# Kernel optimization log

Measured on AMD Instinct MI355X. Metric: run time of the kernel, lower is better.

Reference implementation:

```python
import jax, jax.numpy as jnp
import numpy as np

N_NODES = 100000


def _glorot(key, shape):
    fan_in, fan_out = shape
    lim = (6.0 / (fan_in + fan_out)) ** 0.5
    return jax.random.uniform(key, shape, jnp.float32, -lim, lim)


def setup_inputs() -> dict:
    key = jax.random.key(0)
    ks = jax.random.split(key, 16)
    E = 1600000
    IN, H, OUT = 32, 48, 32
    f = jax.random.normal(ks[0], (N_NODES, IN), jnp.float32)
    edge_index = jax.random.randint(ks[1], (2, E), 0, N_NODES, jnp.int64)
    # layer 1: theta IN->H, phi H->H
    Wt1 = _glorot(ks[2], (IN, H)); bt1 = jnp.zeros((H,), jnp.float32)
    Wp1 = _glorot(ks[3], (H, H));  bp1 = jnp.zeros((H,), jnp.float32)
    # layer 2: theta H->H, phi H->H
    Wt2 = _glorot(ks[4], (H, H)); bt2 = jnp.zeros((H,), jnp.float32)
    Wp2 = _glorot(ks[5], (H, H)); bp2 = jnp.zeros((H,), jnp.float32)
    # layer 3: theta H->OUT, phi OUT->OUT
    Wt3 = _glorot(ks[6], (H, OUT)); bt3 = jnp.zeros((OUT,), jnp.float32)
    Wp3 = _glorot(ks[7], (OUT, OUT)); bp3 = jnp.zeros((OUT,), jnp.float32)
    return {"f": f, "edge_index": edge_index,
            "Wt1": Wt1, "bt1": bt1, "Wp1": Wp1, "bp1": bp1,
            "Wt2": Wt2, "bt2": bt2, "Wp2": Wp2, "bp2": bp2,
            "Wt3": Wt3, "bt3": bt3, "Wp3": Wp3, "bp3": bp3}


def _triconv(f, src, dst, Wt, bt, Wp, bp):
    # message: linear_theta(f_i - f_j), i = target (dst), j = source (src)
    msg = (f[dst] - f[src]) @ Wt + bt          # [E, C_out]
    agg = jax.ops.segment_sum(msg, dst, num_segments=N_NODES)  # sum aggr
    return agg @ Wp + bp                        # linear_phi


def reference(f, edge_index, Wt1, bt1, Wp1, bp1, Wt2, bt2, Wp2, bp2, Wt3, bt3, Wp3, bp3):
    src, dst = edge_index[0], edge_index[1]
    h = jax.nn.relu(_triconv(f, src, dst, Wt1, bt1, Wp1, bp1))
    h = jax.nn.relu(_triconv(h, src, dst, Wt2, bt2, Wp2, bp2))
    out = jax.nn.softmax(_triconv(h, src, dst, Wt3, bt3, Wp3, bp3), axis=-1)
    return out
```

## Files before the change

### kernel.cpp

```cpp
#include <hip/hip_runtime.h>


#define SHIFT 9
#define SPAN 512
#define MAXB 256
#define CHUNK 4096


__global__ void k_detect(const unsigned int* __restrict__ ew,
                         int* __restrict__ flag, int* __restrict__ bcount) {
  int t = threadIdx.x;
  bcount[t] = 0;
  unsigned int v = 0;
#pragma unroll
  for (int j = 0; j < 4; ++j) v |= ew[2 * (t * 4 + j) + 1];
  __shared__ unsigned int red[256];
  red[t] = v;
  __syncthreads();
  for (int s = 128; s > 0; s >>= 1) {
    if (t < s) red[t] |= red[t + s];
    __syncthreads();
  }
  if (t == 0) flag[0] = (red[0] == 0u) ? 1 : 0;
}

__global__ void k_bcount(const void* __restrict__ edges,
                         const int* __restrict__ flag,
                         int* __restrict__ bcount, int E) {
  __shared__ int cnt[MAXB];
  int t = threadIdx.x;
  cnt[t] = 0;
  __syncthreads();
  int base = blockIdx.x * CHUNK;
  if (flag[0]) {
    const long long* p = (const long long*)edges;
#pragma unroll
    for (int j = 0; j < CHUNK / 256; ++j) {
      int idx = base + j * 256 + t;
      if (idx < E) atomicAdd(&cnt[((int)p[E + idx]) >> SHIFT], 1);
    }
  } else {
    const int* p = (const int*)edges;
#pragma unroll
    for (int j = 0; j < CHUNK / 256; ++j) {
      int idx = base + j * 256 + t;
      if (idx < E) atomicAdd(&cnt[p[E + idx] >> SHIFT], 1);
    }
  }
  __syncthreads();
  if (cnt[t]) atomicAdd(&bcount[t], cnt[t]);
}

__global__ void k_bscan(const int* __restrict__ bcount, int* __restrict__ bbase,
                        int* __restrict__ bcursor, int* __restrict__ offs,
                        int NB, int N, int E) {
  __shared__ int lds[MAXB];
  int t = threadIdx.x;
  int v = (t < NB) ? bcount[t] : 0;
  lds[t] = v;
  __syncthreads();
  for (int off = 1; off < MAXB; off <<= 1) {
    int add = (t >= off) ? lds[t - off] : 0;
    __syncthreads();
    lds[t] += add;
    __syncthreads();
  }
  int ex = lds[t] - v;
  bbase[t] = ex;
  bcursor[t] = ex;
  if (t == MAXB - 1) bbase[MAXB] = lds[t];
  if (t == 0) offs[N] = E;
}

__global__ void k_bin(const void* __restrict__ edges,
                      const int* __restrict__ flag, int* __restrict__ bcursor,
                      unsigned int* __restrict__ binned, int E) {
  __shared__ unsigned int pk[CHUNK];
  __shared__ unsigned char bk[CHUNK];
  __shared__ int cnt[MAXB], bb[MAXB], cnt2[MAXB];
  int t = threadIdx.x;
  cnt[t] = 0;
  cnt2[t] = 0;
  __syncthreads();
  int base = blockIdx.x * CHUNK;
  if (flag[0]) {
    const long long* p = (const long long*)edges;
#pragma unroll
    for (int j = 0; j < CHUNK / 256; ++j) {
      int li = j * 256 + t, idx = base + li;
      if (idx < E) {
        int s = (int)p[idx];
        int d = (int)p[E + idx];
        int b = d >> SHIFT;
        pk[li] = ((unsigned)(d & (SPAN - 1)) << 17) | (unsigned)s;
        bk[li] = (unsigned char)b;
        atomicAdd(&cnt[b], 1);
      }
    }
  } else {
    const int* p = (const int*)edges;
#pragma unroll
    for (int j = 0; j < CHUNK / 256; ++j) {
      int li = j * 256 + t, idx = base + li;
      if (idx < E) {
        int s = p[idx];
        int d = p[E + idx];
        int b = d >> SHIFT;
        pk[li] = ((unsigned)(d & (SPAN - 1)) << 17) | (unsigned)s;
        bk[li] = (unsigned char)b;
        atomicAdd(&cnt[b], 1);
      }
    }
  }
  __syncthreads();
  if (cnt[t]) bb[t] = atomicAdd(&bcursor[t], cnt[t]);
  __syncthreads();
#pragma unroll
  for (int j = 0; j < CHUNK / 256; ++j) {
    int li = j * 256 + t, idx = base + li;
    if (idx < E) {
      int b = bk[li];
      int r = atomicAdd(&cnt2[b], 1);
      binned[bb[b] + r] = pk[li];
    }
  }
}

__launch_bounds__(256) __global__
void k_bcsr(const unsigned int* __restrict__ binned,
            const int* __restrict__ bbase, int* __restrict__ offs,
            int* __restrict__ csr, int N) {
  __shared__ int deg[SPAN];
  __shared__ int gs[128];
  __shared__ int cur[SPAN];
  int b = blockIdx.x;
  int t = threadIdx.x;
  deg[t] = 0;
  deg[t + 256] = 0;
  __syncthreads();
  int base = bbase[b];
  int cnt = bbase[b + 1] - base;
  for (int e = t; e < cnt; e += 256)
    atomicAdd(&deg[binned[base + e] >> 17], 1);
  __syncthreads();
  if (t < 128) gs[t] = deg[4 * t] + deg[4 * t + 1] + deg[4 * t + 2] + deg[4 * t + 3];
  __syncthreads();
  for (int off = 1; off < 128; off <<= 1) {
    int add = (t < 128 && t >= off) ? gs[t - off] : 0;
    __syncthreads();
    if (t < 128) gs[t] += add;
    __syncthreads();
  }
  int nodeBase = b << SHIFT;
  if (t < 128) {
    int run = (t == 0) ? 0 : gs[t - 1];
#pragma unroll
    for (int j = 0; j < 4; ++j) {
      int li = 4 * t + j;
      cur[li] = run;
      int node = nodeBase + li;
      if (node < N) offs[node] = base + run;
      run += deg[li];
    }
  }
  __syncthreads();
  for (int e = t; e < cnt; e += 256) {
    unsigned int v = binned[base + e];
    int ld = v >> 17;
    int pos = atomicAdd(&cur[ld], 1);
    csr[base + pos] = (int)(v & 0x1FFFFu);
  }
}

template <int CIN, int COUT, int ACT>
__launch_bounds__(256) __global__
void k_layer(const float* __restrict__ hin, float* __restrict__ hout,
             const int* __restrict__ offs, const int* __restrict__ csr,
             const float* __restrict__ Wt, const float* __restrict__ bt,
             const float* __restrict__ Wp, const float* __restrict__ bp,
             int n) {
  constexpr int NPB = 64;
  constexpr int CH1 = CIN / 4;
  constexpr int NV1 = CH1 / 4;
  constexpr int CH2 = COUT / 4;

  __shared__ float Wtl[CIN * COUT];
  __shared__ float Wpl[COUT * COUT];
  __shared__ float btl[COUT];
  __shared__ float bpl[COUT];
  __shared__ float Tl[NPB][CIN + 4];
  __shared__ float o1l[NPB][COUT + 4];

  int t = threadIdx.x;
  for (int i = t; i < CIN * COUT; i += 256) Wtl[i] = Wt[i];
  for (int i = t; i < COUT * COUT; i += 256) Wpl[i] = Wp[i];
  if (t < COUT) {
    btl[t] = bt[t];
    bpl[t] = bp[t];
  }
  __syncthreads();

  int ln = t >> 2;
  int g = t & 3;
  int node = blockIdx.x * NPB + ln;
  bool valid = node < n;
  int start = valid ? offs[node] : 0;
  int end = valid ? offs[node + 1] : 0;
  float degf = (float)(end - start);

  const int c0 = g * CH1;
  const float* hc = hin + c0;
  float acc[CH1];
#pragma unroll
  for (int j = 0; j < CH1; ++j) acc[j] = 0.f;

  int k = start;
  for (; k + 3 < end; k += 4) {
    int s0 = csr[k], s1 = csr[k + 1], s2 = csr[k + 2], s3 = csr[k + 3];
    float4 v0[NV1], v1[NV1], v2[NV1], v3[NV1];
    const float4* r0 = reinterpret_cast<const float4*>(hc + (size_t)s0 * CIN);
    const float4* r1 = reinterpret_cast<const float4*>(hc + (size_t)s1 * CIN);
    const float4* r2 = reinterpret_cast<const float4*>(hc + (size_t)s2 * CIN);
    const float4* r3 = reinterpret_cast<const float4*>(hc + (size_t)s3 * CIN);
#pragma unroll
    for (int q = 0; q < NV1; ++q) v0[q] = r0[q];
#pragma unroll
    for (int q = 0; q < NV1; ++q) v1[q] = r1[q];
#pragma unroll
    for (int q = 0; q < NV1; ++q) v2[q] = r2[q];
#pragma unroll
    for (int q = 0; q < NV1; ++q) v3[q] = r3[q];
#pragma unroll
    for (int q = 0; q < NV1; ++q) {
      acc[q * 4 + 0] += (v0[q].x + v1[q].x) + (v2[q].x + v3[q].x);
      acc[q * 4 + 1] += (v0[q].y + v1[q].y) + (v2[q].y + v3[q].y);
      acc[q * 4 + 2] += (v0[q].z + v1[q].z) + (v2[q].z + v3[q].z);
      acc[q * 4 + 3] += (v0[q].w + v1[q].w) + (v2[q].w + v3[q].w);
    }
  }
  for (; k < end; ++k) {
    int s0 = csr[k];
    const float4* r0 = reinterpret_cast<const float4*>(hc + (size_t)s0 * CIN);
#pragma unroll
    for (int q = 0; q < NV1; ++q) {
      float4 v = r0[q];
      acc[q * 4 + 0] += v.x;
      acc[q * 4 + 1] += v.y;
      acc[q * 4 + 2] += v.z;
      acc[q * 4 + 3] += v.w;
    }
  }
  if (valid) {
    const float4* me = reinterpret_cast<const float4*>(hc + (size_t)node * CIN);
#pragma unroll
    for (int q = 0; q < NV1; ++q) {
      float4 v = me[q];
      Tl[ln][c0 + q * 4 + 0] = degf * v.x - acc[q * 4 + 0];
      Tl[ln][c0 + q * 4 + 1] = degf * v.y - acc[q * 4 + 1];
      Tl[ln][c0 + q * 4 + 2] = degf * v.z - acc[q * 4 + 2];
      Tl[ln][c0 + q * 4 + 3] = degf * v.w - acc[q * 4 + 3];
    }
  }
  __syncthreads();

  int c2 = g * CH2;
  float a2[CH2];
#pragma unroll
  for (int j = 0; j < CH2; ++j) a2[j] = degf * btl[c2 + j];
#pragma unroll 8
  for (int kk = 0; kk < CIN; ++kk) {
    float tv = Tl[ln][kk];
#pragma unroll
    for (int j = 0; j < CH2; ++j) a2[j] += tv * Wtl[kk * COUT + c2 + j];
  }
#pragma unroll
  for (int j = 0; j < CH2; ++j) o1l[ln][c2 + j] = a2[j];
  __syncthreads();

  float a3[CH2];
#pragma unroll
  for (int j = 0; j < CH2; ++j) a3[j] = bpl[c2 + j];
#pragma unroll 8
  for (int kk = 0; kk < COUT; ++kk) {
    float ov = o1l[ln][kk];
#pragma unroll
    for (int j = 0; j < CH2; ++j) a3[j] += ov * Wpl[kk * COUT + c2 + j];
  }

  if (ACT == 0) {
#pragma unroll
    for (int j = 0; j < CH2; ++j) a3[j] = fmaxf(a3[j], 0.f);
  } else {
    float m = -1e30f;
#pragma unroll
    for (int j = 0; j < CH2; ++j) m = fmaxf(m, a3[j]);
    m = fmaxf(m, __shfl_xor(m, 1));
    m = fmaxf(m, __shfl_xor(m, 2));
    float ssum = 0.f;
#pragma unroll
    for (int j = 0; j < CH2; ++j) {
      a3[j] = __expf(a3[j] - m);
      ssum += a3[j];
    }
    ssum += __shfl_xor(ssum, 1);
    ssum += __shfl_xor(ssum, 2);
    float inv = 1.0f / ssum;
#pragma unroll
    for (int j = 0; j < CH2; ++j) a3[j] *= inv;
  }

  if (valid) {
    float* orow = hout + (size_t)node * COUT + c2;
#pragma unroll
    for (int q = 0; q < CH2 / 4; ++q) {
      reinterpret_cast<float4*>(orow)[q] =
          make_float4(a3[q * 4 + 0], a3[q * 4 + 1], a3[q * 4 + 2], a3[q * 4 + 3]);
    }
  }
}


extern "C" void kernel_launch(void* const* d_in, const int* in_sizes, int n_in,
                              void* d_out, int out_size, void* d_ws,
                              size_t ws_size, hipStream_t stream) {
  const float* f = (const float*)d_in[0];
  const void* edges = d_in[1];
  const float* Wt1 = (const float*)d_in[2];
  const float* bt1 = (const float*)d_in[3];
  const float* Wp1 = (const float*)d_in[4];
  const float* bp1 = (const float*)d_in[5];
  const float* Wt2 = (const float*)d_in[6];
  const float* bt2 = (const float*)d_in[7];
  const float* Wp2 = (const float*)d_in[8];
  const float* bp2 = (const float*)d_in[9];
  const float* Wt3 = (const float*)d_in[10];
  const float* bt3 = (const float*)d_in[11];
  const float* Wp3 = (const float*)d_in[12];
  const float* bp3 = (const float*)d_in[13];

  const int N = in_sizes[0] / 32;
  const int E = in_sizes[1] / 2;
  const int NB = (N + SPAN - 1) >> SHIFT;

  char* ws = (char*)d_ws;
  size_t o = 0;
  auto carve = [&](size_t bytes) {
    size_t r = o;
    o = (o + bytes + 255) & ~(size_t)255;
    return r;
  };
  int* flag = (int*)(ws + carve(256));
  int* bcount = (int*)(ws + carve(MAXB * 4));
  int* bbase = (int*)(ws + carve((MAXB + 1) * 4));
  int* bcursor = (int*)(ws + carve(MAXB * 4));
  int* offs = (int*)(ws + carve((size_t)(N + 1) * 4));
  int* csr = (int*)(ws + carve((size_t)E * 4));
  float* h1 = (float*)(ws + carve((size_t)N * 48 * 4));
  float* h2 = (float*)(ws + carve((size_t)N * 48 * 4));
  unsigned int* binned = (unsigned int*)h1;
  (void)ws_size;

  const int nChunks = (E + CHUNK - 1) / CHUNK;

  k_detect<<<1, 256, 0, stream>>>((const unsigned int*)edges, flag, bcount);
  k_bcount<<<nChunks, 256, 0, stream>>>(edges, flag, bcount, E);
  k_bscan<<<1, 256, 0, stream>>>(bcount, bbase, bcursor, offs, NB, N, E);
  k_bin<<<nChunks, 256, 0, stream>>>(edges, flag, bcursor, binned, E);
  k_bcsr<<<NB, 256, 0, stream>>>(binned, bbase, offs, csr, N);

  const int nbl = (N + 63) / 64;
  k_layer<32, 48, 0><<<nbl, 256, 0, stream>>>(f, h1, offs, csr, Wt1, bt1, Wp1,
                                              bp1, N);
  k_layer<48, 48, 0><<<nbl, 256, 0, stream>>>(h1, h2, offs, csr, Wt2, bt2, Wp2,
                                              bp2, N);
  k_layer<48, 32, 1><<<nbl, 256, 0, stream>>>(h2, (float*)d_out, offs, csr,
                                              Wt3, bt3, Wp3, bp3, N);
}
```

Baseline: 342.8 us.

## Interleave gather channels, replace shared-memory staging with quad shuffles, unroll gather by five

```diff
diff --git a/kernel.cpp b/kernel.cpp
--- a/kernel.cpp
+++ b/kernel.cpp
@@ -173,23 +173,21 @@
 }
 
 template <int CIN, int COUT, int ACT>
-__launch_bounds__(256) __global__
+__launch_bounds__(256, 4) __global__
 void k_layer(const float* __restrict__ hin, float* __restrict__ hout,
              const int* __restrict__ offs, const int* __restrict__ csr,
              const float* __restrict__ Wt, const float* __restrict__ bt,
              const float* __restrict__ Wp, const float* __restrict__ bp,
              int n) {
   constexpr int NPB = 64;
-  constexpr int CH1 = CIN / 4;
-  constexpr int NV1 = CH1 / 4;
+  constexpr int NCK = CIN / 16;
+  constexpr int TCH = NCK * 4;
   constexpr int CH2 = COUT / 4;
 
   __shared__ float Wtl[CIN * COUT];
   __shared__ float Wpl[COUT * COUT];
   __shared__ float btl[COUT];
   __shared__ float bpl[COUT];
-  __shared__ float Tl[NPB][CIN + 4];
-  __shared__ float o1l[NPB][COUT + 4];
 
   int t = threadIdx.x;
   for (int i = t; i < CIN * COUT; i += 256) Wtl[i] = Wt[i];
@@ -208,81 +206,85 @@
   int end = valid ? offs[node + 1] : 0;
   float degf = (float)(end - start);
 
-  const int c0 = g * CH1;
-  const float* hc = hin + c0;
-  float acc[CH1];
-#pragma unroll
-  for (int j = 0; j < CH1; ++j) acc[j] = 0.f;
+  const int fo = 4 * g;
+  float acc[TCH];
+#pragma unroll
+  for (int j = 0; j < TCH; ++j) acc[j] = 0.f;
 
   int k = start;
-  for (; k + 3 < end; k += 4) {
-    int s0 = csr[k], s1 = csr[k + 1], s2 = csr[k + 2], s3 = csr[k + 3];
-    float4 v0[NV1], v1[NV1], v2[NV1], v3[NV1];
-    const float4* r0 = reinterpret_cast<const float4*>(hc + (size_t)s0 * CIN);
-    const float4* r1 = reinterpret_cast<const float4*>(hc + (size_t)s1 * CIN);
-    const float4* r2 = reinterpret_cast<const float4*>(hc + (size_t)s2 * CIN);
-    const float4* r3 = reinterpret_cast<const float4*>(hc + (size_t)s3 * CIN);
-#pragma unroll
-    for (int q = 0; q < NV1; ++q) v0[q] = r0[q];
-#pragma unroll
-    for (int q = 0; q < NV1; ++q) v1[q] = r1[q];
-#pragma unroll
-    for (int q = 0; q < NV1; ++q) v2[q] = r2[q];
-#pragma unroll
-    for (int q = 0; q < NV1; ++q) v3[q] = r3[q];
-#pragma unroll
-    for (int q = 0; q < NV1; ++q) {
-      acc[q * 4 + 0] += (v0[q].x + v1[q].x) + (v2[q].x + v3[q].x);
-      acc[q * 4 + 1] += (v0[q].y + v1[q].y) + (v2[q].y + v3[q].y);
-      acc[q * 4 + 2] += (v0[q].z + v1[q].z) + (v2[q].z + v3[q].z);
-      acc[q * 4 + 3] += (v0[q].w + v1[q].w) + (v2[q].w + v3[q].w);
+  for (; k + 4 < end; k += 5) {
+    int s0 = csr[k], s1 = csr[k + 1], s2 = csr[k + 2], s3 = csr[k + 3],
+        s4 = csr[k + 4];
+    float4 v0[NCK], v1[NCK], v2[NCK], v3[NCK], v4[NCK];
+    const float* r0 = hin + (size_t)s0 * CIN + fo;
+    const float* r1 = hin + (size_t)s1 * CIN + fo;
+    const float* r2 = hin + (size_t)s2 * CIN + fo;
+    const float* r3 = hin + (size_t)s3 * CIN + fo;
+    const float* r4 = hin + (size_t)s4 * CIN + fo;
+#pragma unroll
+    for (int q = 0; q < NCK; ++q) v0[q] = *(const float4*)(r0 + 16 * q);
+#pragma unroll
+    for (int q = 0; q < NCK; ++q) v1[q] = *(const float4*)(r1 + 16 * q);
+#pragma unroll
+    for (int q = 0; q < NCK; ++q) v2[q] = *(const float4*)(r2 + 16 * q);
+#pragma unroll
+    for (int q = 0; q < NCK; ++q) v3[q] = *(const float4*)(r3 + 16 * q);
+#pragma unroll
+    for (int q = 0; q < NCK; ++q) v4[q] = *(const float4*)(r4 + 16 * q);
+#pragma unroll
+    for (int q = 0; q < NCK; ++q) {
+      acc[q * 4 + 0] += (v0[q].x + v1[q].x) + (v2[q].x + v3[q].x) + v4[q].x;
+      acc[q * 4 + 1] += (v0[q].y + v1[q].y) + (v2[q].y + v3[q].y) + v4[q].y;
+      acc[q * 4 + 2] += (v0[q].z + v1[q].z) + (v2[q].z + v3[q].z) + v4[q].z;
+      acc[q * 4 + 3] += (v0[q].w + v1[q].w) + (v2[q].w + v3[q].w) + v4[q].w;
     }
   }
   for (; k < end; ++k) {
-    int s0 = csr[k];
-    const float4* r0 = reinterpret_cast<const float4*>(hc + (size_t)s0 * CIN);
-#pragma unroll
-    for (int q = 0; q < NV1; ++q) {
-      float4 v = r0[q];
+    const float* r0 = hin + (size_t)csr[k] * CIN + fo;
+#pragma unroll
+    for (int q = 0; q < NCK; ++q) {
+      float4 v = *(const float4*)(r0 + 16 * q);
       acc[q * 4 + 0] += v.x;
       acc[q * 4 + 1] += v.y;
       acc[q * 4 + 2] += v.z;
       acc[q * 4 + 3] += v.w;
     }
   }
-  if (valid) {
-    const float4* me = reinterpret_cast<const float4*>(hc + (size_t)node * CIN);
-#pragma unroll
-    for (int q = 0; q < NV1; ++q) {
-      float4 v = me[q];
-      Tl[ln][c0 + q * 4 + 0] = degf * v.x - acc[q * 4 + 0];
-      Tl[ln][c0 + q * 4 + 1] = degf * v.y - acc[q * 4 + 1];
-      Tl[ln][c0 + q * 4 + 2] = degf * v.z - acc[q * 4 + 2];
-      Tl[ln][c0 + q * 4 + 3] = degf * v.w - acc[q * 4 + 3];
-    }
-  }
-  __syncthreads();
-
-  int c2 = g * CH2;
+
+  float tch[TCH];
+  {
+    const float* me = hin + (size_t)(valid ? node : 0) * CIN + fo;
+#pragma unroll
+    for (int q = 0; q < NCK; ++q) {
+      float4 v = *(const float4*)(me + 16 * q);
+      tch[q * 4 + 0] = degf * v.x - acc[q * 4 + 0];
+      tch[q * 4 + 1] = degf * v.y - acc[q * 4 + 1];
+      tch[q * 4 + 2] = degf * v.z - acc[q * 4 + 2];
+      tch[q * 4 + 3] = degf * v.w - acc[q * 4 + 3];
+    }
+  }
+
+  const int c2 = g * CH2;
   float a2[CH2];
 #pragma unroll
   for (int j = 0; j < CH2; ++j) a2[j] = degf * btl[c2 + j];
-#pragma unroll 8
+#pragma unroll
   for (int kk = 0; kk < CIN; ++kk) {
-    float tv = Tl[ln][kk];
+    const int owner = (kk >> 2) & 3;
+    const int idx = ((kk >> 4) << 2) | (kk & 3);
+    float tv = __shfl(tch[idx], owner, 4);
 #pragma unroll
     for (int j = 0; j < CH2; ++j) a2[j] += tv * Wtl[kk * COUT + c2 + j];
   }
-#pragma unroll
-  for (int j = 0; j < CH2; ++j) o1l[ln][c2 + j] = a2[j];
-  __syncthreads();
 
   float a3[CH2];
 #pragma unroll
   for (int j = 0; j < CH2; ++j) a3[j] = bpl[c2 + j];
-#pragma unroll 8
+#pragma unroll
   for (int kk = 0; kk < COUT; ++kk) {
-    float ov = o1l[ln][kk];
+    const int owner = kk / CH2;
+    const int idx = kk % CH2;
+    float ov = __shfl(a2[idx], owner, 4);
 #pragma unroll
     for (int j = 0; j < CH2; ++j) a3[j] += ov * Wpl[kk * COUT + c2 + j];
   }
```

Result: faster. 335.3 us (-2.2%).
